# Kernel optimization log

Measured on AMD Instinct MI355X. Metric: run time of the kernel, lower is better.

The kernel has to match this reference:

```python
import jax, jax.numpy as jnp
import numpy as np

# NSA hyperparams (match init_kwargs)
KS, ST, SEL, TOPN, WIN = 32, 16, 64, 16, 512
NEG = -1e30  # additive mask value (finite so fp32 softmax stays stable)


def setup_inputs() -> dict:
    key = jax.random.key(0)
    ks = jax.random.split(key, 6)
    B, S, Hq, Hk, D, Dv = 1, 2048, 16, 2, 128, 128
    q = jax.random.normal(ks[0], (B, S, Hq, D), jnp.float32)
    k = jax.random.normal(ks[1], (B, S, Hk, D), jnp.float32)
    v = jax.random.normal(ks[2], (B, S, Hk, Dv), jnp.float32)
    # learned per-position compression weights for K and V blocks
    w_cmp_k = jax.random.normal(ks[3], (KS,), jnp.float32) / KS
    w_cmp_v = jax.random.normal(ks[4], (KS,), jnp.float32) / KS
    # gating head: Linear(qk_head_dim, 3) -> sigmoid
    w_gate = jax.random.normal(ks[5], (D, 3), jnp.float32) * 0.02
    b_gate = jnp.zeros((3,), jnp.float32)
    return dict(q=q, k=k, v=v, w_cmp_k=w_cmp_k, w_cmp_v=w_cmp_v,
                w_gate=w_gate, b_gate=b_gate)


def _nsa(q, k, v, w_cmp_k, w_cmp_v, w_gate, b_gate):
    B, S, Hq, D = q.shape
    Hk = k.shape[2]
    G = Hq // Hk                      # GQA group size
    Dv = v.shape[-1]
    scale = D ** -0.5
    t_pos = jnp.arange(S)

    # ---- 1. compressed-KV attention (CompressAttn) ----
    T = (S - KS) // ST + 1            # number of compressed blocks
    widx = jnp.arange(T)[:, None] * ST + jnp.arange(KS)[None, :]   # [T, KS]
    cmp_k = jnp.einsum('btknd,k->btnd', k[:, widx], w_cmp_k)        # [B,T,Hk,D]
    cmp_v = jnp.einsum('btknd,k->btnd', v[:, widx], w_cmp_v)        # [B,T,Hk,Dv]

    qg = q.reshape(B, S, Hk, G, D)
    s_cmp = jnp.einsum('bsngd,btnd->bngst', qg, cmp_k) * scale      # [B,Hk,G,S,T]
    blk_end = jnp.arange(T) * ST + KS - 1
    cmp_mask = blk_end[None, :] <= t_pos[:, None]                   # [S,T] block fully past
    p_cmp = jax.nn.softmax(jnp.where(cmp_mask, s_cmp, NEG), axis=-1)
    p_cmp = p_cmp * cmp_mask          # zero rows with no visible block
    cmp_o = jnp.einsum('bngst,btnd->bsngd', p_cmp, cmp_v).reshape(B, S, Hq, Dv)

    # ---- 2. top-n selection-block scoring (select_for_fwd_bwd) ----
    NSel = S // SEL
    starts = jnp.arange(T) * ST
    b_lo = starts // SEL
    b_hi = (starts + KS - 1) // SEL
    bidx = jnp.arange(NSel)
    # map compressed-block probs onto overlapping selection blocks
    Mmap = ((bidx[None, :] >= b_lo[:, None]) & (bidx[None, :] <= b_hi[:, None])).astype(q.dtype)  # [T,NSel]
    p_slc = jnp.einsum('bngst,tm->bnsm', p_cmp, Mmap)               # sum over group g -> [B,Hk,S,NSel]

    cur_blk = t_pos // SEL
    blk_causal = (bidx[None, :] * SEL) <= t_pos[:, None]            # [S,NSel]
    forced = (bidx[None, :] == 0) | (bidx[None, :] == cur_blk[:, None])
    blk_score = jnp.where(forced, -NEG, p_slc)                      # always keep block 0 + current
    blk_score = jnp.where(blk_causal, blk_score, NEG)
    vals, inds = jax.lax.top_k(blk_score, TOPN)                     # [B,Hk,S,TOPN]
    valid = (vals > NEG / 2).astype(q.dtype)
    sel_blk_mask = (jax.nn.one_hot(inds, NSel, dtype=q.dtype) * valid[..., None]).sum(-2) > 0  # [B,Hk,S,NSel]

    # ---- 3. block-sparse selected attention (select_attn) ----
    tok_sel_mask = jnp.repeat(sel_blk_mask, SEL, axis=-1)           # [B,Hk,S,S]
    causal = t_pos[None, :] <= t_pos[:, None]                       # [S,S]
    tok_sel_mask = tok_sel_mask & causal
    s_tok = jnp.einsum('bsngd,bjnd->bngsj', qg, k) * scale          # [B,Hk,G,S,S] shared scores
    p_sel = jax.nn.softmax(jnp.where(tok_sel_mask[:, :, None], s_tok, NEG), axis=-1)
    sel_o = jnp.einsum('bngsj,bjnd->bsngd', p_sel, v).reshape(B, S, Hq, Dv)

    win_mask = causal & ((t_pos[:, None] - t_pos[None, :]) <= WIN)
    p_win = jax.nn.softmax(jnp.where(win_mask, s_tok, NEG), axis=-1)
    win_o = jnp.einsum('bngsj,bjnd->bsngd', p_win, v).reshape(B, S, Hq, Dv)

    # ---- 5. learned sigmoid gating combine ----
    gate = jax.nn.sigmoid(jnp.einsum('bshd,dc->bshc', q, w_gate) + b_gate)  # [B,S,Hq,3]
    return (cmp_o * gate[..., 0:1] + sel_o * gate[..., 1:2] + win_o * gate[..., 2:3])


def reference(q, k, v, w_cmp_k, w_cmp_v, w_gate, b_gate):
    return _nsa(q, k, v, w_cmp_k, w_cmp_v, w_gate, b_gate)
```

## Files before the change

### kernel.cpp

```cpp
#include <hip/hip_runtime.h>

#define SS   2048
#define HQ   16
#define HK   2
#define GQ   8
#define DD   128
#define DV   128
#define KS   32
#define ST   16
#define SELB 64
#define TOPN 16
#define WINW 512
#define TT   127
#define NSEL 32
#define SCALE 0.08838834764831845f

typedef __attribute__((ext_vector_type(8))) short bf16x8;
typedef __attribute__((ext_vector_type(4))) short short4v;
typedef __attribute__((ext_vector_type(4))) float f32x4;

__device__ __forceinline__ short f2bf(float x) {
    union { float f; unsigned u; } a; a.f = x;
    unsigned r = a.u + 0x7FFFu + ((a.u >> 16) & 1u);
    return (short)(r >> 16);
}
__device__ __forceinline__ float bf2f(short b) {
    union { unsigned u; float f; } x; x.u = ((unsigned)(unsigned short)b) << 16; return x.f;
}

__global__ __launch_bounds__(256) void k_prep(
    const float* __restrict__ k, const float* __restrict__ v,
    const float* __restrict__ wck, const float* __restrict__ wcv,
    short* __restrict__ kfr, short* __restrict__ vfr,
    short* __restrict__ ckh, short* __restrict__ ckl,
    short* __restrict__ cvfr)
{
    __shared__ float red[256];
    int bid = blockIdx.x, tid = threadIdx.x;
    int lane = tid & 63, quad = (lane >> 4) & 3, l16 = lane & 15;
    if (bid < 256) {
        int tb = bid >> 1, n = bid & 1;
        int kb = tid >> 6;
        int token = tb * 16 + l16;
        int feat = kb * 32 + quad * 8;
        const float* src = &k[(token * HK + n) * DD + feat];
        bf16x8 t;
        #pragma unroll
        for (int e = 0; e < 8; ++e) t[e] = f2bf(src[e]);
        *(bf16x8*)&kfr[(((n * 128 + tb) * 4 + kb) * 64 + lane) * 8] = t;
    } else if (bid < 512) {
        int id = bid - 256;
        int cb = id >> 3, n = (id >> 2) & 1, it = id & 3;
        int frag = it * 4 + (tid >> 6);
        int h = frag >> 3, f = frag & 7;
        int d = f * 16 + l16;
        int tok0 = cb * 64 + h * 32 + quad * 8;
        bf16x8 t;
        #pragma unroll
        for (int e = 0; e < 8; ++e) t[e] = f2bf(v[((tok0 + e) * HK + n) * DV + d]);
        *(bf16x8*)&vfr[((((n * 32 + cb) * 2 + h) * 8 + f) * 64 + lane) * 8] = t;
    } else if (bid < 768) {
        int id = bid - 512;
        int n = id & 1, t = id >> 1;
        int d = tid & 127, jh = tid >> 7;
        float a = 0.f;
        if (t < TT) {
            #pragma unroll
            for (int jj = 0; jj < 16; ++jj) {
                int j = jh * 16 + jj;
                a += k[((t * ST + j) * HK + n) * DD + d] * wck[j];
            }
        }
        red[tid] = a;
        __syncthreads();
        if (tid < 128) {
            float s = red[tid] + red[tid + 128];
            short hi = f2bf(s);
            short lo = f2bf(s - bf2f(hi));
            int tile = t >> 4, l16i = t & 15;
            int kb = d >> 5, qd = (d >> 3) & 3, e = d & 7;
            int off = (((n * 8 + tile) * 4 + kb) * 64 + qd * 16 + l16i) * 8 + e;
            ckh[off] = hi;
            ckl[off] = lo;
        }
    } else {
        int id = bid - 768;
        int n = id & 1, tok = id >> 1;
        int d = tid & 127, jh = tid >> 7;
        float a = 0.f;
        if (tok < TT) {
            #pragma unroll
            for (int jj = 0; jj < 16; ++jj) {
                int j = jh * 16 + jj;
                a += v[((tok * ST + j) * HK + n) * DV + d] * wcv[j];
            }
        }
        red[tid] = a;
        __syncthreads();
        if (tid < 128) {
            float s = red[tid] + red[tid + 128];
            int w2 = d >> 5, half = (d >> 4) & 1, l16i = d & 15;
            int kb = tok >> 5, qd = (tok >> 3) & 3, e = tok & 7;
            cvfr[((((n * 4 + w2) * 2 + half) * 4 + kb) * 64 + qd * 16 + l16i) * 8 + e] = f2bf(s);
        }
    }
}

__global__ __launch_bounds__(256, 4) void k_fused(
    const float* __restrict__ q,
    const short* __restrict__ ckh, const short* __restrict__ ckl,
    const short* __restrict__ cvfr,
    const short* __restrict__ kfr, const short* __restrict__ vfr,
    const float* __restrict__ wg, const float* __restrict__ bg,
    float* __restrict__ out)
{
    int s0 = (SS - 2) - (int)blockIdx.x * 2;
    int s1 = s0 + 1;
    int n = blockIdx.y;
    int tid = threadIdx.x;
    int w = tid >> 6, lane = tid & 63, quad = lane >> 4, l16 = lane & 15;

    __shared__ union {
        struct {
            float qs[16][132];
            float p[16][132];
            short Pt[16][136];
        } c;
        struct {
            union {
                short Pw[4][16][64];
                float o_lds[2][16][132];
            } pf;
            short OselB[16][128];
        } f;
    } u;
    __shared__ short cmpO[16][136];
    __shared__ float g3v[16][3];
    __shared__ float pslc2[2][NSEL];
    __shared__ float lw[4][16];
    __shared__ unsigned selMask[2];
    __shared__ unsigned ublk[NSEL];
    __shared__ int shUCnt;

    f32x4 z4 = {0.f, 0.f, 0.f, 0.f};

    for (int i = tid; i < 16 * 128; i += 256) {
        int row = i >> 7, d = i & 127;
        u.c.qs[row][d] = q[((s0 + (row >> 3)) * HQ + n * GQ + (row & 7)) * DD + d];
    }
    __syncthreads();

    bf16x8 qb[4];
    bf16x8 qlb[4];
    {
        const float* qp = &u.c.qs[l16][quad * 8];
        #pragma unroll
        for (int kb = 0; kb < 4; ++kb) {
            f32x4 x = *(const f32x4*)(qp + kb * 32);
            f32x4 y = *(const f32x4*)(qp + kb * 32 + 4);
            bf16x8 th, tl;
            #pragma unroll
            for (int j = 0; j < 4; ++j) {
                th[j] = f2bf(x[j]);     tl[j] = f2bf(x[j] - bf2f(th[j]));
                th[4+j] = f2bf(y[j]);   tl[4+j] = f2bf(y[j] - bf2f(th[4+j]));
            }
            qb[kb] = th; qlb[kb] = tl;
        }
    }
    if (tid < 48) {
        int h2 = tid / 3, c = tid % 3;
        float a = 0.f;
        for (int d2 = 0; d2 < DD; ++d2) a += u.c.qs[h2][d2] * wg[d2 * 3 + c];
        a += bg[c];
        g3v[h2][c] = 1.f / (1.f + __expf(-a));
    }
    for (int tile = w; tile < 8; tile += 4) {
        const short* khp = &ckh[((n * 8 + tile) * 256 + lane) * 8];
        const short* klp = &ckl[((n * 8 + tile) * 256 + lane) * 8];
        f32x4 acc = z4;
        #pragma unroll
        for (int kb = 0; kb < 4; ++kb) {
            bf16x8 ah = *(const bf16x8*)(khp + kb * 512);
            bf16x8 al = *(const bf16x8*)(klp + kb * 512);
            acc = __builtin_amdgcn_mfma_f32_16x16x32_bf16(ah, qb[kb], acc, 0, 0, 0);
            acc = __builtin_amdgcn_mfma_f32_16x16x32_bf16(al, qb[kb], acc, 0, 0, 0);
            acc = __builtin_amdgcn_mfma_f32_16x16x32_bf16(ah, qlb[kb], acc, 0, 0, 0);
        }
        f32x4 sv;
        #pragma unroll
        for (int r = 0; r < 4; ++r) sv[r] = acc[r] * SCALE;
        *(f32x4*)&u.c.p[l16][tile * 16 + quad * 4] = sv;
    }
    __syncthreads();

    int ntt0 = (s0 >= KS - 1) ? min((s0 - (KS - 1)) / ST + 1, TT) : 0;
    int ntt1 = (s1 >= KS - 1) ? min((s1 - (KS - 1)) / ST + 1, TT) : 0;

    #pragma unroll
    for (int rr = 0; rr < 4; ++rr) {
        int row = w * 4 + rr;
        int ntt = (row < 8) ? ntt0 : ntt1;
        int t1 = lane, t2 = lane + 64;
        float v1 = (t1 < ntt) ? u.c.p[row][t1] : -1e30f;
        float v2 = (t2 < ntt) ? u.c.p[row][t2] : -1e30f;
        float m = fmaxf(v1, v2);
        #pragma unroll
        for (int o = 32; o > 0; o >>= 1) m = fmaxf(m, __shfl_xor(m, o, 64));
        float e1 = (t1 < ntt) ? __expf(v1 - m) : 0.f;
        float e2 = (t2 < ntt) ? __expf(v2 - m) : 0.f;
        float ssum = e1 + e2;
        #pragma unroll
        for (int o = 32; o > 0; o >>= 1) ssum += __shfl_xor(ssum, o, 64);
        float inv = (ntt > 0) ? (1.f / ssum) : 0.f;
        e1 *= inv; e2 *= inv;
        u.c.p[row][t1] = e1; u.c.p[row][t2] = e2;
        u.c.Pt[row][t1] = f2bf(e1); u.c.Pt[row][t2] = f2bf(e2);
    }
    __syncthreads();

    if (tid < 64) {
        int p01 = tid >> 5, m = tid & 31;
        float a = 0.f;
        for (int dt = -1; dt < 4; ++dt) {
            int t = 4 * m + dt;
            if (t < 0 || t >= TT) continue;
            bool maps = (t / 4 == m) || ((t % 4 == 3) && (t / 4 == m - 1));
            if (!maps) continue;
            for (int g = 0; g < GQ; ++g) a += u.c.p[p01 * 8 + g][t];
        }
        pslc2[p01][m] = a;
    }
    __syncthreads();

    if (w < 2) {
        int p01 = w;
        int sp = p01 ? s1 : s0;
        int cur = sp / SELB;
        float v;
        if (lane < NSEL) {
            int m = lane;
            if (m == 0 || m == cur) v = 1e30f;
            else if (m * SELB <= sp) v = pslc2[p01][m];
            else v = -1e30f;
        } else v = -1e31f;
        unsigned msk = 0;
        #pragma unroll
        for (int pick = 0; pick < TOPN; ++pick) {
            float bv = v;
            #pragma unroll
            for (int o = 32; o > 0; o >>= 1) bv = fmaxf(bv, __shfl_xor(bv, o, 64));
            unsigned long long b = __ballot(v == bv);
            int best = __ffsll((long long)b) - 1;
            if (bv > -5e29f) msk |= 1u << best;
            if (lane == best) v = -1e31f;
        }
        if (lane == 0) selMask[p01] = msk;
    }
    {
        f32x4 o0 = z4, o1 = z4;
        int d0 = w * 32 + l16;
        const short* cvp = &cvfr[((n * 4 + w) * 512 + lane) * 8];
        #pragma unroll
        for (int kb = 0; kb < 4; ++kb) {
            bf16x8 pa = *(const bf16x8*)&u.c.Pt[l16][kb * 32 + quad * 8];
            bf16x8 vb0 = *(const bf16x8*)(cvp + kb * 512);
            bf16x8 vb1 = *(const bf16x8*)(cvp + 2048 + kb * 512);
            o0 = __builtin_amdgcn_mfma_f32_16x16x32_bf16(pa, vb0, o0, 0, 0, 0);
            o1 = __builtin_amdgcn_mfma_f32_16x16x32_bf16(pa, vb1, o1, 0, 0, 0);
        }
        #pragma unroll
        for (int r = 0; r < 4; ++r) {
            int h2 = quad * 4 + r;
            cmpO[h2][d0]      = f2bf(o0[r]);
            cmpO[h2][d0 + 16] = f2bf(o1[r]);
        }
    }
    __syncthreads();

    if (tid == 0) {
        unsigned m0 = selMask[0], m1 = selMask[1], mu = m0 | m1;
        int uc = 0;
        for (int b = 0; b < NSEL; ++b)
            if ((mu >> b) & 1u)
                ublk[uc++] = (unsigned)(b * SELB) | (((m0 >> b) & 1u) << 30) | (((m1 >> b) & 1u) << 31);
        shUCnt = uc;
    }
    __syncthreads();
    int uCnt = shUCnt;
    int j00 = (s0 >= WINW) ? (s0 - WINW) : 0;
    int j01 = (s1 >= WINW) ? (s1 - WINW) : 0;
    int tb0 = j00 & ~63;
    int nBlkB = ((s1 - tb0) >> 6) + 1;

    int sLim = (l16 < 8) ? s0 : s1;
    f32x4 o[8];
    float lold;

    char* pwRow = (char*)&u.f.pf.Pw[w][l16][0];
    int swz = l16 & 7;

    auto run_chunks = [&](int nB, bool selMode) {
        #pragma unroll
        for (int f = 0; f < 8; ++f) o[f] = z4;
        lold = 0.f;
        int loWin = selMode ? 0 : ((l16 < 8) ? j00 : j01);
        for (int bi = w; bi < nB; bi += 4) {
            int tstart, vis;
            if (selMode) {
                unsigned e = ublk[bi];
                tstart = (int)(e & 0x0FFFFFFFu);
                vis = (l16 < 8) ? (int)((e >> 30) & 1u) : (int)(e >> 31);
            } else {
                tstart = tb0 + bi * 64;
                vis = 1;
            }
            f32x4 a4[4] = {z4, z4, z4, z4};
            {
                const short* kp = &kfr[((n * 128 + (tstart >> 4)) * 256 + lane) * 8];
                bf16x8 kf[2][4];
                #pragma unroll
                for (int t2 = 0; t2 < 2; ++t2)
                    #pragma unroll
                    for (int kb = 0; kb < 4; ++kb)
                        kf[t2][kb] = *(const bf16x8*)(kp + (t2 * 4 + kb) * 512);
                #pragma unroll
                for (int kb = 0; kb < 4; ++kb) {
                    a4[0] = __builtin_amdgcn_mfma_f32_16x16x32_bf16(kf[0][kb], qb[kb], a4[0], 0, 0, 0);
                    a4[1] = __builtin_amdgcn_mfma_f32_16x16x32_bf16(kf[1][kb], qb[kb], a4[1], 0, 0, 0);
                }
                #pragma unroll
                for (int t2 = 0; t2 < 2; ++t2)
                    #pragma unroll
                    for (int kb = 0; kb < 4; ++kb)
                        kf[t2][kb] = *(const bf16x8*)(kp + ((2 + t2) * 4 + kb) * 512);
                #pragma unroll
                for (int kb = 0; kb < 4; ++kb) {
                    a4[2] = __builtin_amdgcn_mfma_f32_16x16x32_bf16(kf[0][kb], qb[kb], a4[2], 0, 0, 0);
                    a4[3] = __builtin_amdgcn_mfma_f32_16x16x32_bf16(kf[1][kb], qb[kb], a4[3], 0, 0, 0);
                }
            }
            const short* vp = &vfr[((n * 32 + (tstart >> 6)) * 1024 + lane) * 8];
            bf16x8 vf[8];
            #pragma unroll
            for (int f = 0; f < 8; ++f) vf[f] = *(const bf16x8*)(vp + f * 512);
            {
                int lo = loWin - tstart;
                int hi = vis ? (sLim - tstart) : (lo - 1);
                int rngS = hi - lo + 1;
                unsigned rng = (unsigned)(rngS > 0 ? rngS : 0);
                int tb = quad * 4 - lo;
                #pragma unroll
                for (int tile = 0; tile < 4; ++tile) {
                    float ev[4];
                    #pragma unroll
                    for (int r = 0; r < 4; ++r) {
                        unsigned uu = (unsigned)(tb + tile * 16 + r);
                        float ex = __expf(a4[tile][r] * SCALE);
                        ev[r] = (uu < rng) ? ex : 0.f;
                    }
                    lold += (ev[0] + ev[1]) + (ev[2] + ev[3]);
                    unsigned plo = (__float_as_uint(ev[1]) & 0xFFFF0000u) | (__float_as_uint(ev[0]) >> 16);
                    unsigned phi = (__float_as_uint(ev[3]) & 0xFFFF0000u) | (__float_as_uint(ev[2]) >> 16);
                    uint2 pk; pk.x = plo; pk.y = phi;
                    int chunk = (tile * 2 + (quad >> 1)) ^ swz;
                    *(uint2*)(pwRow + chunk * 16 + (quad & 1) * 8) = pk;
                }
            }
            __builtin_amdgcn_s_waitcnt(0xC07F);
            bf16x8 pa0 = *(const bf16x8*)(pwRow + ((quad ^ swz) * 16));
            bf16x8 pa1 = *(const bf16x8*)(pwRow + (((4 + quad) ^ swz) * 16));
            #pragma unroll
            for (int f = 0; f < 8; ++f)
                o[f] = __builtin_amdgcn_mfma_f32_16x16x32_bf16(pa0, vf[f], o[f], 0, 0, 0);
            #pragma unroll
            for (int f = 0; f < 8; ++f)
                o[f] = __builtin_amdgcn_mfma_f32_16x16x32_bf16(pa1, *(const bf16x8*)(vp + (8 + f) * 512), o[f], 0, 0, 0);
        }
    };

    auto combine = [&](bool isA) {
        float lsum = lold;
        lsum += __shfl_xor(lsum, 16, 64);
        lsum += __shfl_xor(lsum, 32, 64);
        if (quad == 0) lw[w][l16] = lsum;
        __syncthreads();
        if (w >= 2) {
            #pragma unroll
            for (int f = 0; f < 8; ++f)
                #pragma unroll
                for (int r = 0; r < 4; ++r)
                    u.f.pf.o_lds[w - 2][quad * 4 + r][l16 + 16 * f] = o[f][r];
        }
        __syncthreads();
        float ltot = lw[0][l16] + lw[1][l16] + lw[2][l16] + lw[3][l16];
        float linv = 1.f / ltot;
        float linvr[4];
        #pragma unroll
        for (int r = 0; r < 4; ++r) linvr[r] = __shfl(linv, quad * 4 + r, 64);
        if (w < 2) {
            #pragma unroll
            for (int f = 0; f < 8; ++f)
                #pragma unroll
                for (int r = 0; r < 4; ++r)
                    o[f][r] += u.f.pf.o_lds[w][quad * 4 + r][l16 + 16 * f];
        }
        __syncthreads();
        if (w == 1) {
            #pragma unroll
            for (int f = 0; f < 8; ++f)
                #pragma unroll
                for (int r = 0; r < 4; ++r)
                    u.f.pf.o_lds[0][quad * 4 + r][l16 + 16 * f] = o[f][r];
        }
        __syncthreads();
        if (w == 0) {
            #pragma unroll
            for (int f = 0; f < 8; ++f)
                #pragma unroll
                for (int r = 0; r < 4; ++r)
                    o[f][r] += u.f.pf.o_lds[0][quad * 4 + r][l16 + 16 * f];
            if (isA) {
                #pragma unroll
                for (int f = 0; f < 8; ++f)
                    #pragma unroll
                    for (int r = 0; r < 4; ++r)
                        u.f.OselB[quad * 4 + r][l16 + 16 * f] = f2bf(o[f][r] * linvr[r]);
            } else {
                #pragma unroll
                for (int f = 0; f < 8; ++f)
                    #pragma unroll
                    for (int r = 0; r < 4; ++r) {
                        int h2 = quad * 4 + r;
                        int p = h2 >> 3, g = h2 & 7;
                        int d = l16 + 16 * f;
                        int ob = ((s0 + p) * HQ + n * GQ + g) * DV + d;
                        float owin = o[f][r] * linvr[r];
                        out[ob] = g3v[h2][0] * bf2f(cmpO[h2][d]) + g3v[h2][1] * bf2f(u.f.OselB[h2][d]) + g3v[h2][2] * owin;
                    }
            }
        }
        __syncthreads();
    };

    run_chunks(uCnt, true);
    combine(true);
    run_chunks(nBlkB, false);
    combine(false);
}

extern "C" void kernel_launch(void* const* d_in, const int* in_sizes, int n_in,
                              void* d_out, int out_size, void* d_ws, size_t ws_size,
                              hipStream_t stream) {
    const float* q   = (const float*)d_in[0];
    const float* k   = (const float*)d_in[1];
    const float* v   = (const float*)d_in[2];
    const float* wck = (const float*)d_in[3];
    const float* wcv = (const float*)d_in[4];
    const float* wg  = (const float*)d_in[5];
    const float* bg  = (const float*)d_in[6];
    float* out = (float*)d_out;

    short* kfr  = (short*)d_ws;
    short* vfr  = kfr + 2 * 128 * 4 * 64 * 8;
    short* ckh  = vfr + 2 * 32 * 2 * 8 * 64 * 8;
    short* ckl  = ckh + 2 * 8 * 4 * 64 * 8;
    short* cvfr = ckl + 2 * 8 * 4 * 64 * 8;

    k_prep<<<1024, 256, 0, stream>>>(k, v, wck, wcv, kfr, vfr, ckh, ckl, cvfr);
    k_fused<<<dim3(SS / 2, HK), 256, 0, stream>>>(q, ckh, ckl, cvfr, kfr, vfr, wg, bg, out);
}
```

Before: 170.9 us.

## Feed P·V MFMA directly from registers using 16x16x16 bf16 ops

```diff
diff --git a/kernel.cpp b/kernel.cpp
--- a/kernel.cpp
+++ b/kernel.cpp
@@ -18,6 +18,19 @@
 typedef __attribute__((ext_vector_type(8))) short bf16x8;
 typedef __attribute__((ext_vector_type(4))) short short4v;
 typedef __attribute__((ext_vector_type(4))) float f32x4;
+
+#if defined(__has_builtin)
+#if __has_builtin(__builtin_amdgcn_mfma_f32_16x16x16bf16_1k)
+#define MFMA16(a, b, c) __builtin_amdgcn_mfma_f32_16x16x16bf16_1k(a, b, c, 0, 0, 0)
+#endif
+#endif
+#ifndef MFMA16
+static __device__ __forceinline__ f32x4 mfma16_asm(short4v a, short4v b, f32x4 c) {
+    asm volatile("v_mfma_f32_16x16x16_bf16 %0, %1, %2, %0" : "+v"(c) : "v"(a), "v"(b));
+    return c;
+}
+#define MFMA16(a, b, c) mfma16_asm(a, b, c)
+#endif
 
 __device__ __forceinline__ short f2bf(float x) {
     union { float f; unsigned u; } a; a.f = x;
@@ -51,14 +64,17 @@
     } else if (bid < 512) {
         int id = bid - 256;
         int cb = id >> 3, n = (id >> 2) & 1, it = id & 3;
-        int frag = it * 4 + (tid >> 6);
-        int h = frag >> 3, f = frag & 7;
-        int d = f * 16 + l16;
-        int tok0 = cb * 64 + h * 32 + quad * 8;
-        bf16x8 t;
-        #pragma unroll
-        for (int e = 0; e < 8; ++e) t[e] = f2bf(v[((tok0 + e) * HK + n) * DV + d]);
-        *(bf16x8*)&vfr[((((n * 32 + cb) * 2 + h) * 8 + f) * 64 + lane) * 8] = t;
+        #pragma unroll
+        for (int rep = 0; rep < 2; ++rep) {
+            int p = it * 8 + (tid >> 6) * 2 + rep;
+            int st = p >> 3, f = p & 7;
+            int d = f * 16 + l16;
+            int tok0 = cb * 64 + st * 16 + quad * 4;
+            short4v t;
+            #pragma unroll
+            for (int e = 0; e < 4; ++e) t[e] = f2bf(v[((tok0 + e) * HK + n) * DV + d]);
+            *(short4v*)&vfr[((((n * 32 + cb) * 4 + st) * 8 + f) * 64 + lane) * 4] = t;
+        }
     } else if (bid < 768) {
         int id = bid - 512;
         int n = id & 1, t = id >> 1;
@@ -127,10 +143,7 @@
             short Pt[16][136];
         } c;
         struct {
-            union {
-                short Pw[4][16][64];
-                float o_lds[2][16][132];
-            } pf;
+            float o_lds[2][16][132];
             short OselB[16][128];
         } f;
     } u;
@@ -296,9 +309,6 @@
     f32x4 o[8];
     float lold;
 
-    char* pwRow = (char*)&u.f.pf.Pw[w][l16][0];
-    int swz = l16 & 7;
-
     auto run_chunks = [&](int nB, bool selMode) {
         #pragma unroll
         for (int f = 0; f < 8; ++f) o[f] = z4;
@@ -339,10 +349,7 @@
                     a4[3] = __builtin_amdgcn_mfma_f32_16x16x32_bf16(kf[1][kb], qb[kb], a4[3], 0, 0, 0);
                 }
             }
-            const short* vp = &vfr[((n * 32 + (tstart >> 6)) * 1024 + lane) * 8];
-            bf16x8 vf[8];
-            #pragma unroll
-            for (int f = 0; f < 8; ++f) vf[f] = *(const bf16x8*)(vp + f * 512);
+            short4v ps[4];
             {
                 int lo = loWin - tstart;
                 int hi = vis ? (sLim - tstart) : (lo - 1);
@@ -359,22 +366,22 @@
                         ev[r] = (uu < rng) ? ex : 0.f;
                     }
                     lold += (ev[0] + ev[1]) + (ev[2] + ev[3]);
-                    unsigned plo = (__float_as_uint(ev[1]) & 0xFFFF0000u) | (__float_as_uint(ev[0]) >> 16);
-                    unsigned phi = (__float_as_uint(ev[3]) & 0xFFFF0000u) | (__float_as_uint(ev[2]) >> 16);
-                    uint2 pk; pk.x = plo; pk.y = phi;
-                    int chunk = (tile * 2 + (quad >> 1)) ^ swz;
-                    *(uint2*)(pwRow + chunk * 16 + (quad & 1) * 8) = pk;
+                    union { uint2 u2; short4v s4; } pk;
+                    pk.u2.x = (__float_as_uint(ev[1]) & 0xFFFF0000u) | (__float_as_uint(ev[0]) >> 16);
+                    pk.u2.y = (__float_as_uint(ev[3]) & 0xFFFF0000u) | (__float_as_uint(ev[2]) >> 16);
+                    ps[tile] = pk.s4;
                 }
             }
-            __builtin_amdgcn_s_waitcnt(0xC07F);
-            bf16x8 pa0 = *(const bf16x8*)(pwRow + ((quad ^ swz) * 16));
-            bf16x8 pa1 = *(const bf16x8*)(pwRow + (((4 + quad) ^ swz) * 16));
-            #pragma unroll
-            for (int f = 0; f < 8; ++f)
-                o[f] = __builtin_amdgcn_mfma_f32_16x16x32_bf16(pa0, vf[f], o[f], 0, 0, 0);
-            #pragma unroll
-            for (int f = 0; f < 8; ++f)
-                o[f] = __builtin_amdgcn_mfma_f32_16x16x32_bf16(pa1, *(const bf16x8*)(vp + (8 + f) * 512), o[f], 0, 0, 0);
+            const short* vp2 = &vfr[(size_t)(n * 32 + (tstart >> 6)) * 8192 + lane * 4];
+            #pragma unroll
+            for (int st = 0; st < 4; ++st) {
+                const short* vs = vp2 + st * 2048;
+                #pragma unroll
+                for (int f = 0; f < 8; ++f) {
+                    short4v vb = *(const short4v*)(vs + f * 256);
+                    o[f] = MFMA16(ps[st], vb, o[f]);
+                }
+            }
         }
     };
 
@@ -389,7 +396,7 @@
             for (int f = 0; f < 8; ++f)
                 #pragma unroll
                 for (int r = 0; r < 4; ++r)
-                    u.f.pf.o_lds[w - 2][quad * 4 + r][l16 + 16 * f] = o[f][r];
+                    u.f.o_lds[w - 2][quad * 4 + r][l16 + 16 * f] = o[f][r];
         }
         __syncthreads();
         float ltot = lw[0][l16] + lw[1][l16] + lw[2][l16] + lw[3][l16];
@@ -402,7 +409,7 @@
             for (int f = 0; f < 8; ++f)
                 #pragma unroll
                 for (int r = 0; r < 4; ++r)
-                    o[f][r] += u.f.pf.o_lds[w][quad * 4 + r][l16 + 16 * f];
+                    o[f][r] += u.f.o_lds[w][quad * 4 + r][l16 + 16 * f];
         }
         __syncthreads();
         if (w == 1) {
@@ -410,7 +417,7 @@
             for (int f = 0; f < 8; ++f)
                 #pragma unroll
                 for (int r = 0; r < 4; ++r)
-                    u.f.pf.o_lds[0][quad * 4 + r][l16 + 16 * f] = o[f][r];
+                    u.f.o_lds[0][quad * 4 + r][l16 + 16 * f] = o[f][r];
         }
         __syncthreads();
         if (w == 0) {
@@ -418,7 +425,7 @@
             for (int f = 0; f < 8; ++f)
                 #pragma unroll
                 for (int r = 0; r < 4; ++r)
-                    o[f][r] += u.f.pf.o_lds[0][quad * 4 + r][l16 + 16 * f];
+                    o[f][r] += u.f.o_lds[0][quad * 4 + r][l16 + 16 * f];
             if (isA) {
                 #pragma unroll
                 for (int f = 0; f < 8; ++f)
@@ -462,7 +469,7 @@
 
     short* kfr  = (short*)d_ws;
     short* vfr  = kfr + 2 * 128 * 4 * 64 * 8;
-    short* ckh  = vfr + 2 * 32 * 2 * 8 * 64 * 8;
+    short* ckh  = vfr + 2 * 32 * 4 * 8 * 64 * 4;
     short* ckl  = ckh + 2 * 8 * 4 * 64 * 8;
     short* cvfr = ckl + 2 * 8 * 4 * 64 * 8;
 
```

Measured after the change: 203.3 us. +18.9%, slower.

## Fold softmax scale into Q with exp2, compute row sums via MFMA, parallelize gate

Applied to the files above, without the earlier changes.

```diff
diff --git a/kernel.cpp b/kernel.cpp
--- a/kernel.cpp
+++ b/kernel.cpp
@@ -13,11 +13,19 @@
 #define WINW 512
 #define TT   127
 #define NSEL 32
-#define SCALE 0.08838834764831845f
+#define QSC  0.12751744f
 
 typedef __attribute__((ext_vector_type(8))) short bf16x8;
-typedef __attribute__((ext_vector_type(4))) short short4v;
 typedef __attribute__((ext_vector_type(4))) float f32x4;
+
+#if defined(__has_builtin)
+#  if __has_builtin(__builtin_amdgcn_exp2f)
+#    define EXP2(x) __builtin_amdgcn_exp2f(x)
+#  endif
+#endif
+#ifndef EXP2
+#  define EXP2(x) __expf((x) * 0.6931471805599453f)
+#endif
 
 __device__ __forceinline__ short f2bf(float x) {
     union { float f; unsigned u; } a; a.f = x;
@@ -143,6 +151,7 @@
     __shared__ int shUCnt;
 
     f32x4 z4 = {0.f, 0.f, 0.f, 0.f};
+    const bf16x8 ones8 = {0x3F80, 0x3F80, 0x3F80, 0x3F80, 0x3F80, 0x3F80, 0x3F80, 0x3F80};
 
     for (int i = tid; i < 16 * 128; i += 256) {
         int row = i >> 7, d = i & 127;
@@ -161,18 +170,12 @@
             bf16x8 th, tl;
             #pragma unroll
             for (int j = 0; j < 4; ++j) {
-                th[j] = f2bf(x[j]);     tl[j] = f2bf(x[j] - bf2f(th[j]));
-                th[4+j] = f2bf(y[j]);   tl[4+j] = f2bf(y[j] - bf2f(th[4+j]));
+                float xs = x[j] * QSC, ys = y[j] * QSC;
+                th[j] = f2bf(xs);     tl[j] = f2bf(xs - bf2f(th[j]));
+                th[4+j] = f2bf(ys);   tl[4+j] = f2bf(ys - bf2f(th[4+j]));
             }
             qb[kb] = th; qlb[kb] = tl;
         }
-    }
-    if (tid < 48) {
-        int h2 = tid / 3, c = tid % 3;
-        float a = 0.f;
-        for (int d2 = 0; d2 < DD; ++d2) a += u.c.qs[h2][d2] * wg[d2 * 3 + c];
-        a += bg[c];
-        g3v[h2][c] = 1.f / (1.f + __expf(-a));
     }
     for (int tile = w; tile < 8; tile += 4) {
         const short* khp = &ckh[((n * 8 + tile) * 256 + lane) * 8];
@@ -186,10 +189,7 @@
             acc = __builtin_amdgcn_mfma_f32_16x16x32_bf16(al, qb[kb], acc, 0, 0, 0);
             acc = __builtin_amdgcn_mfma_f32_16x16x32_bf16(ah, qlb[kb], acc, 0, 0, 0);
         }
-        f32x4 sv;
-        #pragma unroll
-        for (int r = 0; r < 4; ++r) sv[r] = acc[r] * SCALE;
-        *(f32x4*)&u.c.p[l16][tile * 16 + quad * 4] = sv;
+        *(f32x4*)&u.c.p[l16][tile * 16 + quad * 4] = acc;
     }
     __syncthreads();
 
@@ -206,8 +206,8 @@
         float m = fmaxf(v1, v2);
         #pragma unroll
         for (int o = 32; o > 0; o >>= 1) m = fmaxf(m, __shfl_xor(m, o, 64));
-        float e1 = (t1 < ntt) ? __expf(v1 - m) : 0.f;
-        float e2 = (t2 < ntt) ? __expf(v2 - m) : 0.f;
+        float e1 = (t1 < ntt) ? EXP2(v1 - m) : 0.f;
+        float e2 = (t2 < ntt) ? EXP2(v2 - m) : 0.f;
         float ssum = e1 + e2;
         #pragma unroll
         for (int o = 32; o > 0; o >>= 1) ssum += __shfl_xor(ssum, o, 64);
@@ -277,6 +277,7 @@
     }
     __syncthreads();
 
+    float* gpart = &u.c.p[0][0];
     if (tid == 0) {
         unsigned m0 = selMask[0], m1 = selMask[1], mu = m0 | m1;
         int uc = 0;
@@ -284,8 +285,23 @@
             if ((mu >> b) & 1u)
                 ublk[uc++] = (unsigned)(b * SELB) | (((m0 >> b) & 1u) << 30) | (((m1 >> b) & 1u) << 31);
         shUCnt = uc;
-    }
-    __syncthreads();
+    } else if (tid >= 64) {
+        int t2 = tid - 64;
+        int h2 = t2 / 12, rem = t2 % 12;
+        int c = rem >> 2, qtr = rem & 3;
+        const float* qrow = &u.c.qs[h2][qtr * 32];
+        float a = 0.f;
+        #pragma unroll
+        for (int d2 = 0; d2 < 32; ++d2) a += qrow[d2] * wg[(qtr * 32 + d2) * 3 + c];
+        gpart[t2] = a;
+    }
+    __syncthreads();
+    if (tid < 48) {
+        int h2 = tid / 3, c = tid % 3;
+        int base = h2 * 12 + c * 4;
+        float a = gpart[base] + gpart[base + 1] + gpart[base + 2] + gpart[base + 3] + bg[c];
+        g3v[h2][c] = 1.f / (1.f + __expf(-a));
+    }
     int uCnt = shUCnt;
     int j00 = (s0 >= WINW) ? (s0 - WINW) : 0;
     int j01 = (s1 >= WINW) ? (s1 - WINW) : 0;
@@ -294,7 +310,7 @@
 
     int sLim = (l16 < 8) ? s0 : s1;
     f32x4 o[8];
-    float lold;
+    f32x4 lacc;
 
     char* pwRow = (char*)&u.f.pf.Pw[w][l16][0];
     int swz = l16 & 7;
@@ -302,7 +318,7 @@
     auto run_chunks = [&](int nB, bool selMode) {
         #pragma unroll
         for (int f = 0; f < 8; ++f) o[f] = z4;
-        lold = 0.f;
+        lacc = z4;
         int loWin = selMode ? 0 : ((l16 < 8) ? j00 : j01);
         for (int bi = w; bi < nB; bi += 4) {
             int tstart, vis;
@@ -355,10 +371,9 @@
                     #pragma unroll
                     for (int r = 0; r < 4; ++r) {
                         unsigned uu = (unsigned)(tb + tile * 16 + r);
-                        float ex = __expf(a4[tile][r] * SCALE);
+                        float ex = EXP2(a4[tile][r]);
                         ev[r] = (uu < rng) ? ex : 0.f;
                     }
-                    lold += (ev[0] + ev[1]) + (ev[2] + ev[3]);
                     unsigned plo = (__float_as_uint(ev[1]) & 0xFFFF0000u) | (__float_as_uint(ev[0]) >> 16);
                     unsigned phi = (__float_as_uint(ev[3]) & 0xFFFF0000u) | (__float_as_uint(ev[2]) >> 16);
                     uint2 pk; pk.x = plo; pk.y = phi;
@@ -369,6 +384,8 @@
             __builtin_amdgcn_s_waitcnt(0xC07F);
             bf16x8 pa0 = *(const bf16x8*)(pwRow + ((quad ^ swz) * 16));
             bf16x8 pa1 = *(const bf16x8*)(pwRow + (((4 + quad) ^ swz) * 16));
+            lacc = __builtin_amdgcn_mfma_f32_16x16x32_bf16(pa0, ones8, lacc, 0, 0, 0);
+            lacc = __builtin_amdgcn_mfma_f32_16x16x32_bf16(pa1, ones8, lacc, 0, 0, 0);
             #pragma unroll
             for (int f = 0; f < 8; ++f)
                 o[f] = __builtin_amdgcn_mfma_f32_16x16x32_bf16(pa0, vf[f], o[f], 0, 0, 0);
@@ -379,10 +396,10 @@
     };
 
     auto combine = [&](bool isA) {
-        float lsum = lold;
-        lsum += __shfl_xor(lsum, 16, 64);
-        lsum += __shfl_xor(lsum, 32, 64);
-        if (quad == 0) lw[w][l16] = lsum;
+        if (l16 == 0) {
+            #pragma unroll
+            for (int r = 0; r < 4; ++r) lw[w][quad * 4 + r] = lacc[r];
+        }
         __syncthreads();
         if (w >= 2) {
             #pragma unroll
```

Result: no change. 168.0 us (-1.7%).
